# Kernel tuning notes

Measured on AMD Instinct MI355X. Metric: run time of the kernel, lower is better.

## Reference

```python
import jax, jax.numpy as jnp
import numpy as np
from jax import lax


def _conv1(y, w):
    # y: (B, C) channel vector; w: (3,) Conv1d kernel (cross-correlation, pad=1, no bias)
    yp = jnp.pad(y, ((0, 0), (1, 1)))
    return w[0] * yp[:, :-2] + w[1] * yp[:, 1:-1] + w[2] * yp[:, 2:]


def _scale_branch(xs, dw_w, dw_b, ca_w, ra_w, gate_w, gate_b):
    # xs: (B, C, h, w) one scale of the multi-scale token map
    B, C = xs.shape[0], xs.shape[1]
    xs = lax.conv_general_dilated(
        xs, dw_w, (1, 1), 'SAME', feature_group_count=C,
        dimension_numbers=('NCHW', 'OIHW', 'NCHW')) + dw_b[None, :, None, None]
    avg = xs.mean(axis=(2, 3))          # (B, C) == AdaptiveAvgPool2d(1)
    mx = xs.max(axis=(2, 3))            # (B, C) == AdaptiveMaxPool2d(1)
    gw = jax.nn.softmax(avg @ gate_w + gate_b, axis=1)  # (B, 2) gating over experts
    pooled = avg + mx
    ca_s = jax.nn.sigmoid(_conv1(pooled, ca_w))          # CA channel gate
    ra_s = 1.0 - jax.nn.sigmoid(_conv1(pooled, ra_w))    # RA reverse gate
    # blend the two SE-style experts per channel, then broadcast-multiply
    scale = gw[:, 0:1] * ca_s + gw[:, 1:2] * ra_s        # (B, C)
    out = xs * scale[:, :, None, None]
    return out.reshape(B, C, -1).transpose(0, 2, 1)      # (B, h*w, C)


def setup_inputs() -> dict:
    key = jax.random.key(0)
    ks = jax.random.split(key, 12)
    B, N, Cin, Ch = 8, 5376, 384, 768
    s = lambda k, shape, fan: jax.random.normal(k, shape, jnp.float32) * (1.0 / np.sqrt(fan))
    return {
        'x': jax.random.normal(ks[0], (B, N, Cin), jnp.float32),
        'fc1_w': s(ks[1], (Cin, Ch), Cin),
        'fc1_b': jnp.zeros((Ch,), jnp.float32),
        'dw_w': s(ks[2], (Ch, 1, 3, 3), 9),
        'dw_b': jnp.zeros((Ch,), jnp.float32),
        'ca_w': s(ks[3], (3,), 3),
        'ra_w': s(ks[4], (3,), 3),
        'gate_w': s(ks[5], (Ch, 2), Ch),
        'gate_b': jnp.zeros((2,), jnp.float32),
        'fc2_w': s(ks[6], (Ch, Cin), Ch),
        'fc2_b': jnp.zeros((Cin,), jnp.float32),
        'H': 32,
        'W': 32,
    }


def reference(x, fc1_w, fc1_b, dw_w, dw_b, ca_w, ra_w, gate_w, gate_b, fc2_w, fc2_b, H, W):
    B, N, _ = x.shape
    C = fc1_w.shape[1]
    h = x @ fc1_w + fc1_b                     # fc1: (B, N, C)
    n = N // 21
    to_map = lambda seg, hh, ww: seg.transpose(0, 2, 1).reshape(B, C, hh, ww)
    x1 = to_map(h[:, :16 * n], 2 * H, 2 * W)
    x2 = to_map(h[:, 16 * n:20 * n], H, W)
    x3 = to_map(h[:, 20 * n:], H // 2, W // 2)
    parts = [_scale_branch(xi, dw_w, dw_b, ca_w, ra_w, gate_w, gate_b)
             for xi in (x1, x2, x3)]
    h = jnp.concatenate(parts, axis=1)        # (B, N, C)
    h = jax.nn.gelu(h, approximate=False)     # torch nn.GELU default = exact erf
    return h @ fc2_w + fc2_b
```

## Files before the change

### kernel.cpp

```cpp
#include <hip/hip_runtime.h>
#include <math.h>

#define B_   8
#define NTOK 5376
#define CIN  384
#define CH   768
#define M_   (B_*NTOK)

typedef unsigned short u16;
typedef unsigned int   u32;

using bf16x8 = __attribute__((ext_vector_type(8))) short;
using bf16x4 = __attribute__((ext_vector_type(4))) short;
using f32x4  = __attribute__((ext_vector_type(4))) float;

__device__ __forceinline__ u16 f2bf(float f) {
    union { float f; u32 u; } v; v.f = f;
    u32 r = v.u + 0x7fffu + ((v.u >> 16) & 1u);
    return (u16)(r >> 16);
}
__device__ __forceinline__ float bf2f(u16 u) {
    union { u32 u; float f; } v; v.u = ((u32)u) << 16;
    return v.f;
}

__global__ void k_cvt_x(const float* __restrict__ x, u16* __restrict__ xb, int n4) {
    int i = blockIdx.x * blockDim.x + threadIdx.x;
    if (i >= n4) return;
    float4 v = ((const float4*)x)[i];
    ushort4 o;
    o.x = f2bf(v.x); o.y = f2bf(v.y); o.z = f2bf(v.z); o.w = f2bf(v.w);
    ((ushort4*)xb)[i] = o;
}

__global__ void k_cvt_wT(const float* __restrict__ w, u16* __restrict__ wT, int K, int N) {
    int i = blockIdx.x * blockDim.x + threadIdx.x;
    if (i >= N * K) return;
    int n = i / K, k = i % K;
    wT[i] = f2bf(w[k * N + n]);
}

#define BM 128
#define BN 128
#define BK 64

template<bool OUT_BF16>
__launch_bounds__(256)
__global__ void gemm_bf16_kernel(const u16* __restrict__ A, const u16* __restrict__ Bt,
                                 const float* __restrict__ bias, void* __restrict__ Cout,
                                 int M, int N, int K) {
    __shared__ __align__(16) u16 sA[BM * BK];
    __shared__ __align__(16) u16 sB[BN * BK];
    const int mt = blockIdx.x, nt = blockIdx.y;
    const int tid = threadIdx.x;
    const int wave = tid >> 6, lane = tid & 63;
    const int wm = wave >> 1, wn = wave & 1;
    const int row0 = mt * BM, col0 = nt * BN;
    const int lr = lane & 15, lk = lane >> 4;

    f32x4 acc[4][4];
#pragma unroll
    for (int m = 0; m < 4; m++)
#pragma unroll
        for (int n = 0; n < 4; n++) acc[m][n] = (f32x4){0.f, 0.f, 0.f, 0.f};

    const int KT = K / BK;
    for (int kt = 0; kt < KT; ++kt) {
        const int k0 = kt * BK;
#pragma unroll
        for (int it = 0; it < 4; ++it) {
            int g  = it * 256 + tid;
            int r  = g >> 3;
            int ks = g & 7;
            const u16* gA = A + (size_t)(row0 + r) * K + k0 + ks * 8;
            const u16* gB = Bt + (size_t)(col0 + r) * K + k0 + ks * 8;
            u16* lA = sA + (size_t)(it * 256 + wave * 64) * 8;
            u16* lB = sB + (size_t)(it * 256 + wave * 64) * 8;
            __builtin_amdgcn_global_load_lds(
                (const __attribute__((address_space(1))) u32*)(const void*)gA,
                (__attribute__((address_space(3))) u32*)(void*)lA, 16, 0, 0);
            __builtin_amdgcn_global_load_lds(
                (const __attribute__((address_space(1))) u32*)(const void*)gB,
                (__attribute__((address_space(3))) u32*)(void*)lB, 16, 0, 0);
        }
        __syncthreads();
#pragma unroll
        for (int kk = 0; kk < 2; ++kk) {
            bf16x8 af[4], bfr[4];
#pragma unroll
            for (int m = 0; m < 4; m++)
                af[m] = *(const bf16x8*)&sA[(wm * 64 + m * 16 + lr) * BK + kk * 32 + lk * 8];
#pragma unroll
            for (int n = 0; n < 4; n++)
                bfr[n] = *(const bf16x8*)&sB[(wn * 64 + n * 16 + lr) * BK + kk * 32 + lk * 8];
#pragma unroll
            for (int m = 0; m < 4; m++)
#pragma unroll
                for (int n = 0; n < 4; n++)
                    acc[m][n] = __builtin_amdgcn_mfma_f32_16x16x32_bf16(af[m], bfr[n], acc[m][n], 0, 0, 0);
        }
        __syncthreads();
    }

#pragma unroll
    for (int m = 0; m < 4; m++) {
#pragma unroll
        for (int n = 0; n < 4; n++) {
            int col = col0 + wn * 64 + n * 16 + lr;
            float bv = bias[col];
#pragma unroll
            for (int r = 0; r < 4; r++) {
                int row = row0 + wm * 64 + m * 16 + lk * 4 + r;
                float v = acc[m][n][r] + bv;
                if (OUT_BF16)
                    ((u16*)Cout)[(size_t)row * N + col] = f2bf(v);
                else
                    ((float*)Cout)[(size_t)row * N + col] = v;
            }
        }
    }
}

__launch_bounds__(192)
__global__ void k_conv(const u16* __restrict__ h, const float* __restrict__ dw_w,
                       const float* __restrict__ dw_b, u16* __restrict__ xs,
                       float* __restrict__ psum, float* __restrict__ pmax) {
    const int xflat = blockIdx.x, b = blockIdx.y;
    int x, tokbase, LW;
    if (xflat < 64)      { x = xflat;      tokbase = 0;    LW = 6; }
    else if (xflat < 96) { x = xflat - 64; tokbase = 4096; LW = 5; }
    else                 { x = xflat - 96; tokbase = 5120; LW = 4; }
    const int W = 1 << LW, H = W;
    const int c4 = threadIdx.x, c0 = c4 * 4;

    float wv[3][3][4], dwb[4];
#pragma unroll
    for (int j = 0; j < 4; j++) {
        dwb[j] = dw_b[c0 + j];
#pragma unroll
        for (int t = 0; t < 9; t++) wv[t / 3][t % 3][j] = dw_w[(c0 + j) * 9 + t];
    }

    const size_t colbase = ((size_t)(b * NTOK + tokbase + x)) * CH + c0;
    const int RS = W * CH;
    const bool xm = (x > 0), xp = (x < W - 1);
    const bf16x4 z4 = (bf16x4){0, 0, 0, 0};

    bf16x4 r0[3], r1[3], r2[3];
#pragma unroll
    for (int cidx = 0; cidx < 3; cidx++) r0[cidx] = z4;
    r1[0] = xm ? *(const bf16x4*)&h[colbase - CH] : z4;
    r1[1] = *(const bf16x4*)&h[colbase];
    r1[2] = xp ? *(const bf16x4*)&h[colbase + CH] : z4;

    float as[4] = {0.f, 0.f, 0.f, 0.f};
    float am[4] = {-3.4e38f, -3.4e38f, -3.4e38f, -3.4e38f};

#pragma unroll 2
    for (int y = 0; y < H; ++y) {
        if (y + 1 < H) {
            size_t rb = colbase + (size_t)(y + 1) * RS;
            r2[0] = xm ? *(const bf16x4*)&h[rb - CH] : z4;
            r2[1] = *(const bf16x4*)&h[rb];
            r2[2] = xp ? *(const bf16x4*)&h[rb + CH] : z4;
        } else {
            r2[0] = z4; r2[1] = z4; r2[2] = z4;
        }
        float o[4];
#pragma unroll
        for (int j = 0; j < 4; j++) o[j] = dwb[j];
#pragma unroll
        for (int cidx = 0; cidx < 3; cidx++) {
#pragma unroll
            for (int j = 0; j < 4; j++) {
                o[j] += wv[0][cidx][j] * bf2f((u16)r0[cidx][j]);
                o[j] += wv[1][cidx][j] * bf2f((u16)r1[cidx][j]);
                o[j] += wv[2][cidx][j] * bf2f((u16)r2[cidx][j]);
            }
        }
        bf16x4 ov;
#pragma unroll
        for (int j = 0; j < 4; j++) {
            ov[j] = (short)f2bf(o[j]);
            as[j] += o[j];
            am[j] = fmaxf(am[j], o[j]);
        }
        *(bf16x4*)&xs[colbase + (size_t)y * RS] = ov;
#pragma unroll
        for (int cidx = 0; cidx < 3; cidx++) { r0[cidx] = r1[cidx]; r1[cidx] = r2[cidx]; }
    }

    float4 s4 = make_float4(as[0], as[1], as[2], as[3]);
    float4 m4 = make_float4(am[0], am[1], am[2], am[3]);
    size_t pidx = ((size_t)xflat * 8 + b) * CH + c0;
    *(float4*)&psum[pidx] = s4;
    *(float4*)&pmax[pidx] = m4;
}

__global__ void k_scale(const float* __restrict__ psum, const float* __restrict__ pmax,
                        const float* __restrict__ gate_w, const float* __restrict__ gate_b,
                        const float* __restrict__ ca_w, const float* __restrict__ ra_w,
                        float* __restrict__ scale) {
    int s = blockIdx.x, b = blockIdx.y;
    int tid = threadIdx.x;
    int slot0  = (s == 0) ? 0 : (s == 1) ? 64 : 96;
    int nslots = (s == 0) ? 64 : (s == 1) ? 32 : 16;
    float npos = (s == 0) ? 4096.f : (s == 1) ? 1024.f : 256.f;
    __shared__ float pooled[CH];
    __shared__ float rl[4][2];
    float l0 = 0.f, l1 = 0.f;
#pragma unroll
    for (int j = 0; j < 3; j++) {
        int c = j * 256 + tid;
        float smv = 0.f, mxv = -3.4e38f;
        for (int t = 0; t < nslots; t++) {
            size_t idx = ((size_t)(slot0 + t) * 8 + b) * CH + c;
            smv += psum[idx];
            mxv = fmaxf(mxv, pmax[idx]);
        }
        float avg = smv / npos;
        pooled[c] = avg + mxv;
        l0 += avg * gate_w[c * 2 + 0];
        l1 += avg * gate_w[c * 2 + 1];
    }
    for (int off = 32; off; off >>= 1) {
        l0 += __shfl_down(l0, off);
        l1 += __shfl_down(l1, off);
    }
    int wave = tid >> 6, lane = tid & 63;
    if (lane == 0) { rl[wave][0] = l0; rl[wave][1] = l1; }
    __syncthreads();
    float L0 = rl[0][0] + rl[1][0] + rl[2][0] + rl[3][0] + gate_b[0];
    float L1 = rl[0][1] + rl[1][1] + rl[2][1] + rl[3][1] + gate_b[1];
    float mxl = fmaxf(L0, L1);
    float e0 = expf(L0 - mxl), e1 = expf(L1 - mxl);
    float g0 = e0 / (e0 + e1), g1 = e1 / (e0 + e1);
    float cw0 = ca_w[0], cw1 = ca_w[1], cw2 = ca_w[2];
    float rw0 = ra_w[0], rw1 = ra_w[1], rw2 = ra_w[2];
#pragma unroll
    for (int j = 0; j < 3; j++) {
        int c = j * 256 + tid;
        float pm = (c > 0)      ? pooled[c - 1] : 0.f;
        float pc = pooled[c];
        float pp = (c < CH - 1) ? pooled[c + 1] : 0.f;
        float cas = 1.f / (1.f + expf(-(cw0 * pm + cw1 * pc + cw2 * pp)));
        float ras = 1.f - 1.f / (1.f + expf(-(rw0 * pm + rw1 * pc + rw2 * pp)));
        scale[((size_t)s * 8 + b) * CH + c] = g0 * cas + g1 * ras;
    }
}

#define NG (M_ * (CH / 8))
__global__ void k_apply(u16* __restrict__ xs, const float* __restrict__ scale) {
    for (int gi = blockIdx.x * blockDim.x + threadIdx.x; gi < NG;
         gi += gridDim.x * blockDim.x) {
        int c8 = gi % 96;
        int tl = gi / 96;
        int t = tl % NTOK, b = tl / NTOK;
        int s = (t < 4096) ? 0 : (t < 5120 ? 1 : 2);
        const float4* sp = (const float4*)&scale[((size_t)(s * 8 + b)) * CH + c8 * 8];
        float4 sc0 = sp[0], sc1 = sp[1];
        float scv[8] = {sc0.x, sc0.y, sc0.z, sc0.w, sc1.x, sc1.y, sc1.z, sc1.w};
        bf16x8 v = *(const bf16x8*)&xs[(size_t)gi * 8];
        bf16x8 o;
#pragma unroll
        for (int j = 0; j < 8; j++) {
            float f = bf2f((u16)v[j]) * scv[j];
            float gl = 0.5f * f * (1.f + erff(f * 0.70710678118654752f));
            o[j] = (short)f2bf(gl);
        }
        *(bf16x8*)&xs[(size_t)gi * 8] = o;
    }
}

extern "C" void kernel_launch(void* const* d_in, const int* in_sizes, int n_in,
                              void* d_out, int out_size, void* d_ws, size_t ws_size,
                              hipStream_t stream) {
    const float* x      = (const float*)d_in[0];
    const float* fc1_w  = (const float*)d_in[1];
    const float* fc1_b  = (const float*)d_in[2];
    const float* dw_w   = (const float*)d_in[3];
    const float* dw_b   = (const float*)d_in[4];
    const float* ca_w   = (const float*)d_in[5];
    const float* ra_w   = (const float*)d_in[6];
    const float* gate_w = (const float*)d_in[7];
    const float* gate_b = (const float*)d_in[8];
    const float* fc2_w  = (const float*)d_in[9];
    const float* fc2_b  = (const float*)d_in[10];

    char* ws = (char*)d_ws;
    u16*  xb    = (u16*)(ws);
    u16*  hb    = (u16*)(ws + 33030144);
    u16*  xs    = (u16*)(ws + 99090432);
    u16*  w1T   = (u16*)(ws + 165150720);
    u16*  w2T   = (u16*)(ws + 165740544);
    float* psum = (float*)(ws);
    float* pmax = (float*)(ws + 2752512);
    float* scale= (float*)(ws + 5505024);

    k_cvt_x<<<16128, 256, 0, stream>>>(x, xb, (M_ * CIN) / 4);
    k_cvt_wT<<<(CIN * CH + 255) / 256, 256, 0, stream>>>(fc1_w, w1T, CIN, CH);
    k_cvt_wT<<<(CIN * CH + 255) / 256, 256, 0, stream>>>(fc2_w, w2T, CH, CIN);

    gemm_bf16_kernel<true><<<dim3(M_ / BM, CH / BN), 256, 0, stream>>>(
        xb, w1T, fc1_b, (void*)hb, M_, CH, CIN);

    k_conv<<<dim3(112, 8), 192, 0, stream>>>(hb, dw_w, dw_b, xs, psum, pmax);

    k_scale<<<dim3(3, 8), 256, 0, stream>>>(psum, pmax, gate_w, gate_b, ca_w, ra_w, scale);

    k_apply<<<4096, 256, 0, stream>>>(xs, scale);

    gemm_bf16_kernel<false><<<dim3(M_ / BM, CIN / BN), 256, 0, stream>>>(
        xs, w2T, fc2_b, d_out, M_, CIN, CH);
}
```

Baseline: 373.4 us.

## Tile depthwise conv into 8x8 spatial blocks with atomic pooled reductions

```diff
diff --git a/kernel.cpp b/kernel.cpp
--- a/kernel.cpp
+++ b/kernel.cpp
@@ -23,14 +23,27 @@
     union { u32 u; float f; } v; v.u = ((u32)u) << 16;
     return v.f;
 }
-
-__global__ void k_cvt_x(const float* __restrict__ x, u16* __restrict__ xb, int n4) {
+__device__ __forceinline__ u32 fkey(float f) {
+    union { float f; u32 u; } v; v.f = f;
+    return (v.u & 0x80000000u) ? ~v.u : (v.u | 0x80000000u);
+}
+__device__ __forceinline__ float fkeyinv(u32 k) {
+    union { u32 u; float f; } v;
+    v.u = (k & 0x80000000u) ? (k ^ 0x80000000u) : ~k;
+    return v.f;
+}
+
+__global__ void k_cvt_x(const float* __restrict__ x, u16* __restrict__ xb, int n8) {
     int i = blockIdx.x * blockDim.x + threadIdx.x;
-    if (i >= n4) return;
-    float4 v = ((const float4*)x)[i];
-    ushort4 o;
-    o.x = f2bf(v.x); o.y = f2bf(v.y); o.z = f2bf(v.z); o.w = f2bf(v.w);
-    ((ushort4*)xb)[i] = o;
+    if (i >= n8) return;
+    float4 a = ((const float4*)x)[2 * i];
+    float4 b = ((const float4*)x)[2 * i + 1];
+    bf16x8 o;
+    o[0] = (short)f2bf(a.x); o[1] = (short)f2bf(a.y);
+    o[2] = (short)f2bf(a.z); o[3] = (short)f2bf(a.w);
+    o[4] = (short)f2bf(b.x); o[5] = (short)f2bf(b.y);
+    o[6] = (short)f2bf(b.z); o[7] = (short)f2bf(b.w);
+    ((bf16x8*)xb)[i] = o;
 }
 
 __global__ void k_cvt_wT(const float* __restrict__ w, u16* __restrict__ wT, int K, int N) {
@@ -124,87 +137,97 @@
 __launch_bounds__(192)
 __global__ void k_conv(const u16* __restrict__ h, const float* __restrict__ dw_w,
                        const float* __restrict__ dw_b, u16* __restrict__ xs,
-                       float* __restrict__ psum, float* __restrict__ pmax) {
-    const int xflat = blockIdx.x, b = blockIdx.y;
-    int x, tokbase, LW;
-    if (xflat < 64)      { x = xflat;      tokbase = 0;    LW = 6; }
-    else if (xflat < 96) { x = xflat - 64; tokbase = 4096; LW = 5; }
-    else                 { x = xflat - 96; tokbase = 5120; LW = 4; }
+                       float* __restrict__ psum, u32* __restrict__ pmaxk) {
+    const int tile = blockIdx.x, b = blockIdx.y;
+    int s, xt, yt, tokbase, LW;
+    if (tile < 64)      { s = 0; xt = tile & 7;  yt = tile >> 3; tokbase = 0;    LW = 6; }
+    else if (tile < 80) { int u = tile - 64; s = 1; xt = u & 3; yt = u >> 2; tokbase = 4096; LW = 5; }
+    else                { int u = tile - 80; s = 2; xt = u & 1; yt = u >> 1; tokbase = 5120; LW = 4; }
     const int W = 1 << LW, H = W;
-    const int c4 = threadIdx.x, c0 = c4 * 4;
-
-    float wv[3][3][4], dwb[4];
+    const int x0 = xt * 8, y0 = yt * 8;
+    const int c0 = threadIdx.x * 4;
+
+    float wv[9][4], dwb[4];
 #pragma unroll
     for (int j = 0; j < 4; j++) {
         dwb[j] = dw_b[c0 + j];
 #pragma unroll
-        for (int t = 0; t < 9; t++) wv[t / 3][t % 3][j] = dw_w[(c0 + j) * 9 + t];
-    }
-
-    const size_t colbase = ((size_t)(b * NTOK + tokbase + x)) * CH + c0;
-    const int RS = W * CH;
-    const bool xm = (x > 0), xp = (x < W - 1);
+        for (int t = 0; t < 9; t++) wv[t][j] = dw_w[(c0 + j) * 9 + t];
+    }
+
+    const size_t base = ((size_t)(b * NTOK + tokbase)) * CH + c0;
     const bf16x4 z4 = (bf16x4){0, 0, 0, 0};
-
-    bf16x4 r0[3], r1[3], r2[3];
-#pragma unroll
-    for (int cidx = 0; cidx < 3; cidx++) r0[cidx] = z4;
-    r1[0] = xm ? *(const bf16x4*)&h[colbase - CH] : z4;
-    r1[1] = *(const bf16x4*)&h[colbase];
-    r1[2] = xp ? *(const bf16x4*)&h[colbase + CH] : z4;
+    bool colv[10];
+    int coloff[10];
+#pragma unroll
+    for (int j = 0; j < 10; j++) {
+        int xx = x0 - 1 + j;
+        colv[j] = (xx >= 0) && (xx < W);
+        coloff[j] = xx * CH;
+    }
+
+    bf16x4 r[3][10];
+
+#define LOADROW(slot, yrow) {                                                   \
+        int yr_ = (yrow);                                                       \
+        bool rv_ = ((unsigned)yr_ < (unsigned)H);                               \
+        int rb_ = yr_ * W * CH;                                                 \
+        _Pragma("unroll")                                                       \
+        for (int j = 0; j < 10; j++)                                            \
+            r[slot][j] = (rv_ && colv[j]) ? *(const bf16x4*)&h[base + rb_ + coloff[j]] : z4; \
+    }
+
+    LOADROW(0, y0 - 1);
+    LOADROW(1, y0);
 
     float as[4] = {0.f, 0.f, 0.f, 0.f};
     float am[4] = {-3.4e38f, -3.4e38f, -3.4e38f, -3.4e38f};
 
-#pragma unroll 2
-    for (int y = 0; y < H; ++y) {
-        if (y + 1 < H) {
-            size_t rb = colbase + (size_t)(y + 1) * RS;
-            r2[0] = xm ? *(const bf16x4*)&h[rb - CH] : z4;
-            r2[1] = *(const bf16x4*)&h[rb];
-            r2[2] = xp ? *(const bf16x4*)&h[rb + CH] : z4;
-        } else {
-            r2[0] = z4; r2[1] = z4; r2[2] = z4;
-        }
-        float o[4];
-#pragma unroll
-        for (int j = 0; j < 4; j++) o[j] = dwb[j];
-#pragma unroll
-        for (int cidx = 0; cidx < 3; cidx++) {
+#pragma unroll
+    for (int yy = 0; yy < 8; ++yy) {
+        const int sm1 = yy % 3, sc = (yy + 1) % 3, sp1 = (yy + 2) % 3;
+        LOADROW(sp1, y0 + yy + 1);
+        const int orow = (y0 + yy) * W * CH;
+#pragma unroll
+        for (int p = 0; p < 8; ++p) {
+            float o[4];
+#pragma unroll
+            for (int j = 0; j < 4; j++) o[j] = dwb[j];
+#pragma unroll
+            for (int kx = 0; kx < 3; ++kx) {
+                const int ci = p + kx;
+#pragma unroll
+                for (int j = 0; j < 4; j++) {
+                    o[j] += wv[0 + kx][j] * bf2f((u16)r[sm1][ci][j]);
+                    o[j] += wv[3 + kx][j] * bf2f((u16)r[sc ][ci][j]);
+                    o[j] += wv[6 + kx][j] * bf2f((u16)r[sp1][ci][j]);
+                }
+            }
+            bf16x4 ov;
 #pragma unroll
             for (int j = 0; j < 4; j++) {
-                o[j] += wv[0][cidx][j] * bf2f((u16)r0[cidx][j]);
-                o[j] += wv[1][cidx][j] * bf2f((u16)r1[cidx][j]);
-                o[j] += wv[2][cidx][j] * bf2f((u16)r2[cidx][j]);
+                ov[j] = (short)f2bf(o[j]);
+                as[j] += o[j];
+                am[j] = fmaxf(am[j], o[j]);
             }
-        }
-        bf16x4 ov;
-#pragma unroll
-        for (int j = 0; j < 4; j++) {
-            ov[j] = (short)f2bf(o[j]);
-            as[j] += o[j];
-            am[j] = fmaxf(am[j], o[j]);
-        }
-        *(bf16x4*)&xs[colbase + (size_t)y * RS] = ov;
-#pragma unroll
-        for (int cidx = 0; cidx < 3; cidx++) { r0[cidx] = r1[cidx]; r1[cidx] = r2[cidx]; }
-    }
-
-    float4 s4 = make_float4(as[0], as[1], as[2], as[3]);
-    float4 m4 = make_float4(am[0], am[1], am[2], am[3]);
-    size_t pidx = ((size_t)xflat * 8 + b) * CH + c0;
-    *(float4*)&psum[pidx] = s4;
-    *(float4*)&pmax[pidx] = m4;
-}
-
-__global__ void k_scale(const float* __restrict__ psum, const float* __restrict__ pmax,
+            *(bf16x4*)&xs[base + orow + (x0 + p) * CH] = ov;
+        }
+    }
+#undef LOADROW
+
+#pragma unroll
+    for (int j = 0; j < 4; j++) {
+        atomicAdd(&psum[(s * 8 + b) * CH + c0 + j], as[j]);
+        atomicMax(&pmaxk[(s * 8 + b) * CH + c0 + j], fkey(am[j]));
+    }
+}
+
+__global__ void k_scale(const float* __restrict__ psum, const u32* __restrict__ pmaxk,
                         const float* __restrict__ gate_w, const float* __restrict__ gate_b,
                         const float* __restrict__ ca_w, const float* __restrict__ ra_w,
                         float* __restrict__ scale) {
     int s = blockIdx.x, b = blockIdx.y;
     int tid = threadIdx.x;
-    int slot0  = (s == 0) ? 0 : (s == 1) ? 64 : 96;
-    int nslots = (s == 0) ? 64 : (s == 1) ? 32 : 16;
     float npos = (s == 0) ? 4096.f : (s == 1) ? 1024.f : 256.f;
     __shared__ float pooled[CH];
     __shared__ float rl[4][2];
@@ -212,13 +235,9 @@
 #pragma unroll
     for (int j = 0; j < 3; j++) {
         int c = j * 256 + tid;
-        float smv = 0.f, mxv = -3.4e38f;
-        for (int t = 0; t < nslots; t++) {
-            size_t idx = ((size_t)(slot0 + t) * 8 + b) * CH + c;
-            smv += psum[idx];
-            mxv = fmaxf(mxv, pmax[idx]);
-        }
-        float avg = smv / npos;
+        size_t idx = ((size_t)s * 8 + b) * CH + c;
+        float avg = psum[idx] / npos;
+        float mxv = fkeyinv(pmaxk[idx]);
         pooled[c] = avg + mxv;
         l0 += avg * gate_w[c * 2 + 0];
         l1 += avg * gate_w[c * 2 + 1];
@@ -293,20 +312,22 @@
     u16*  xs    = (u16*)(ws + 99090432);
     u16*  w1T   = (u16*)(ws + 165150720);
     u16*  w2T   = (u16*)(ws + 165740544);
-    float* psum = (float*)(ws);
-    float* pmax = (float*)(ws + 2752512);
-    float* scale= (float*)(ws + 5505024);
-
-    k_cvt_x<<<16128, 256, 0, stream>>>(x, xb, (M_ * CIN) / 4);
+    float* psum = (float*)(ws + 166330368);
+    u32*  pmaxk = (u32*)(ws + 166404096);
+    float* scale= (float*)(ws + 166477824);
+
+    hipMemsetAsync((void*)psum, 0, 147456, stream);
+
+    k_cvt_x<<<(M_ * CIN / 8 + 255) / 256, 256, 0, stream>>>(x, xb, M_ * CIN / 8);
     k_cvt_wT<<<(CIN * CH + 255) / 256, 256, 0, stream>>>(fc1_w, w1T, CIN, CH);
     k_cvt_wT<<<(CIN * CH + 255) / 256, 256, 0, stream>>>(fc2_w, w2T, CH, CIN);
 
     gemm_bf16_kernel<true><<<dim3(M_ / BM, CH / BN), 256, 0, stream>>>(
         xb, w1T, fc1_b, (void*)hb, M_, CH, CIN);
 
-    k_conv<<<dim3(112, 8), 192, 0, stream>>>(hb, dw_w, dw_b, xs, psum, pmax);
-
-    k_scale<<<dim3(3, 8), 256, 0, stream>>>(psum, pmax, gate_w, gate_b, ca_w, ra_w, scale);
+    k_conv<<<dim3(84, 8), 192, 0, stream>>>(hb, dw_w, dw_b, xs, psum, pmaxk);
+
+    k_scale<<<dim3(3, 8), 256, 0, stream>>>(psum, pmaxk, gate_w, gate_b, ca_w, ra_w, scale);
 
     k_apply<<<4096, 256, 0, stream>>>(xs, scale);
 
```

New measurement: 336.7 us. 1.11x faster.
